# Kernel tuning notes

Measured on AMD Instinct MI355X. Metric: run time of the kernel, lower is better.

Reference implementation:

```python
import jax, jax.numpy as jnp
import numpy as np

B, S, DM, TD, H, HD = 2, 2048, 1024, 1024, 16, 64


def setup_inputs() -> dict:
    key = jax.random.key(0)
    k1, k2, k3, k4 = jax.random.split(key, 4)
    query = jax.random.normal(k1, (B, S, DM), dtype=jnp.float32)
    # fused QKV projection weight (nn.Linear weight layout: [out, in]) and output proj
    W_in = jax.random.normal(k2, (3 * TD, DM), dtype=jnp.float32) * 0.02
    W_out = jax.random.normal(k3, (DM, TD), dtype=jnp.float32) * 0.02
    # standard RoPE tables, broadcastable against [B, H, S, HD]
    inv_freq = 1.0 / (10000.0 ** (jnp.arange(0, HD, 2, dtype=jnp.float32) / HD))
    t = jnp.arange(S, dtype=jnp.float32)
    freqs = jnp.outer(t, inv_freq)                      # [S, HD/2]
    emb = jnp.concatenate([freqs, freqs], axis=-1)      # [S, HD]
    sin_q = jnp.sin(emb)[None, None]                    # [1,1,S,HD]
    cos_q = jnp.cos(emb)[None, None]
    # padding mask over keys: first length[b] positions valid (>= S/2 so no NaN rows)
    lengths = jax.random.randint(k4, (B,), S // 2, S + 1)
    attn_mask = jnp.arange(S)[None, :] < lengths[:, None]  # [B, S] bool
    return {"query": query, "W_in": W_in, "W_out": W_out,
            "sin_q": sin_q, "cos_q": cos_q, "attn_mask": attn_mask}


def _rotate_half(x):
    x1, x2 = jnp.split(x, 2, axis=-1)
    return jnp.concatenate([-x2, x1], axis=-1)


def reference(query, W_in, W_out, sin_q, cos_q, attn_mask):
    # fused QKV projection (proj_in, bias=False)
    qkv = query @ W_in.T                                # [B, S, 3*TD]
    q, k, v = jnp.split(qkv, 3, axis=-1)
    to_heads = lambda x: x.reshape(B, S, H, HD).transpose(0, 2, 1, 3)  # [B,H,S,HD]
    q, k, v = to_heads(q), to_heads(k), to_heads(v)
    # RoPE (prefix = 0 since sin covers full sequence)
    q = q * cos_q + _rotate_half(q) * sin_q
    k = k * cos_q + _rotate_half(k) * sin_q
    # SDPA with padding-mask bias + causal mask
    scale = 1.0 / jnp.sqrt(jnp.float32(HD))
    scores = jnp.einsum('bhqd,bhkd->bhqk', q, k) * scale  # [B,H,S,S]
    causal = jnp.arange(S)[:, None] >= jnp.arange(S)[None, :]  # [S, S]
    mask = attn_mask[:, None, None, :] & causal[None, None]    # [B,1,S,S]
    scores = jnp.where(mask, scores, -jnp.inf)
    attn = jax.nn.softmax(scores, axis=-1)
    out = jnp.einsum('bhqk,bhkd->bhqd', attn, v)        # [B,H,S,HD]
    out = out.transpose(0, 2, 1, 3).reshape(B, S, TD)
    return out @ W_out.T                                 # [B, S, DM]
```

## Files before the change

kernel.cpp:

```cpp
#include <hip/hip_runtime.h>
#include <hip/hip_bf16.h>

#define B_ 2
#define S_ 2048
#define DM_ 1024
#define TD_ 1024
#define H_ 16
#define HD_ 64

using bf16 = __hip_bfloat16;
typedef __attribute__((ext_vector_type(8))) short s8v;
typedef __attribute__((ext_vector_type(4))) float f4v;

__device__ __forceinline__ f4v mfma_bf16(s8v a, s8v b, f4v c) {
    return __builtin_amdgcn_mfma_f32_16x16x32_bf16(a, b, c, 0, 0, 0);
}

__device__ __forceinline__ unsigned cvt_pk_bf16(float a, float b) {
    unsigned r;
    asm("v_cvt_pk_bf16_f32 %0, %1, %2" : "=v"(r) : "v"(a), "v"(b));
    return r;
}
__device__ __forceinline__ int2 pack4bf(float a, float b, float c, float d) {
    int2 r;
    r.x = (int)cvt_pk_bf16(a, b);
    r.y = (int)cvt_pk_bf16(c, d);
    return r;
}

__device__ __forceinline__ bool detect_f32(const unsigned int* __restrict__ cosw) {
    return (cosw[0] & 0xFFFFu) == 0u;
}

__device__ __forceinline__ float ld_f(const void* p, int idx, bool f32) {
    return f32 ? ((const float*)p)[idx]
               : __bfloat162float(((const bf16*)p)[idx]);
}

__device__ __forceinline__ void gload_lds16(const bf16* g, void* l) {
    __builtin_amdgcn_global_load_lds(
        (const __attribute__((address_space(1))) unsigned int*)(const void*)g,
        (__attribute__((address_space(3))) unsigned int*)l,
        16, 0, 0);
}

#define NQ_  (B_ * S_ * DM_)
#define NWI_ (3 * TD_ * DM_)
#define NWO_ (DM_ * TD_)
#define NCVT_BLOCKS ((NQ_ + NWI_ + NWO_) / 2048)

__global__ __launch_bounds__(256)
void prep_all(const void* __restrict__ q, const void* __restrict__ wi,
              const void* __restrict__ wo, bf16* __restrict__ dst,
              const void* __restrict__ mask, int* __restrict__ lengths,
              const unsigned int* __restrict__ cosw) {
    const int bid = blockIdx.x;
    if (bid < NCVT_BLOCKS) {
        const bool f32 = detect_f32(cosw);
        int i = (bid * 256 + threadIdx.x) * 8;
        const void* src; int off;
        if (i < NQ_)              { src = q;  off = i; }
        else if (i < NQ_ + NWI_)  { src = wi; off = i - NQ_; }
        else                      { src = wo; off = i - NQ_ - NWI_; }
        if (f32) {
            const float* p = (const float*)src + off;
            float4 x = *reinterpret_cast<const float4*>(p);
            float4 y = *reinterpret_cast<const float4*>(p + 4);
            union { unsigned u[4]; int4 v; } t;
            t.u[0] = cvt_pk_bf16(x.x, x.y);
            t.u[1] = cvt_pk_bf16(x.z, x.w);
            t.u[2] = cvt_pk_bf16(y.x, y.y);
            t.u[3] = cvt_pk_bf16(y.z, y.w);
            *reinterpret_cast<int4*>(dst + i) = t.v;
        } else {
            *reinterpret_cast<int4*>(dst + i) =
                *reinterpret_cast<const int4*>((const bf16*)src + off);
        }
        return;
    }
    int b = bid - NCVT_BLOCKS;
    unsigned int w0 = ((const unsigned int*)mask)[0];
    int enc;
    if (w0 == 1u) enc = 0;
    else if (w0 == 0x01010101u) enc = 1;
    else if (w0 == 0x3F803F80u) enc = 2;
    else enc = 3;
    int cnt = 0;
    for (int s = threadIdx.x; s < S_; s += 256) {
        int i = b * S_ + s;
        bool v;
        if (enc == 0)      v = ((const int*)mask)[i] != 0;
        else if (enc == 1) v = ((const unsigned char*)mask)[i] != 0;
        else if (enc == 2) v = ((const unsigned short*)mask)[i] != 0;
        else               v = ((const float*)mask)[i] != 0.f;
        cnt += v ? 1 : 0;
    }
    __shared__ int red[256];
    red[threadIdx.x] = cnt;
    __syncthreads();
    for (int off = 128; off > 0; off >>= 1) {
        if (threadIdx.x < off) red[threadIdx.x] += red[threadIdx.x + off];
        __syncthreads();
    }
    if (threadIdx.x == 0) lengths[b] = red[0];
}

__global__ __launch_bounds__(256)
void gemm_nt(const bf16* __restrict__ A, const bf16* __restrict__ Bm,
             void* __restrict__ C, int M, int N, int K,
             int c_dyn, const unsigned int* __restrict__ cosw) {
    __shared__ bf16 lds_a[128 * 64];
    __shared__ bf16 lds_b[128 * 64];

    const bool cf32 = c_dyn && detect_f32(cosw);

    const int t = threadIdx.x;
    const int wave = t >> 6, lane = t & 63;
    const int quad = lane >> 4, l16 = lane & 15;
    const int wm = wave >> 1, wn = wave & 1;
    const int m0 = blockIdx.y * 128, n0 = blockIdx.x * 128;
    const int wuni = __builtin_amdgcn_readfirstlane(wave);

    f4v acc[4][4];
    #pragma unroll
    for (int i = 0; i < 4; i++)
        #pragma unroll
        for (int j = 0; j < 4; j++)
            acc[i][j] = f4v{0.f, 0.f, 0.f, 0.f};

    for (int k0 = 0; k0 < K; k0 += 64) {
        __syncthreads();
        #pragma unroll
        for (int i = 0; i < 4; i++) {
            int ci = i * 256 + t;
            int row = ci >> 3;
            int csrc = (ci & 7) ^ (row & 7);
            gload_lds16(A + (size_t)(m0 + row) * K + k0 + csrc * 8,
                        (char*)lds_a + i * 4096 + wuni * 1024);
            gload_lds16(Bm + (size_t)(n0 + row) * K + k0 + csrc * 8,
                        (char*)lds_b + i * 4096 + wuni * 1024);
        }
        __syncthreads();

        #pragma unroll
        for (int kk = 0; kk < 2; kk++) {
            s8v afr[4], bfr[4];
            #pragma unroll
            for (int mb = 0; mb < 4; mb++) {
                int r = wm * 64 + mb * 16 + l16;
                int ch = (kk * 4 + quad) ^ (l16 & 7);
                afr[mb] = *reinterpret_cast<const s8v*>(&lds_a[r * 64 + ch * 8]);
            }
            #pragma unroll
            for (int nb = 0; nb < 4; nb++) {
                int r = wn * 64 + nb * 16 + l16;
                int ch = (kk * 4 + quad) ^ (l16 & 7);
                bfr[nb] = *reinterpret_cast<const s8v*>(&lds_b[r * 64 + ch * 8]);
            }
            #pragma unroll
            for (int mb = 0; mb < 4; mb++)
                #pragma unroll
                for (int nb = 0; nb < 4; nb++)
                    acc[mb][nb] = mfma_bf16(bfr[nb], afr[mb], acc[mb][nb]);
        }
    }

    #pragma unroll
    for (int mb = 0; mb < 4; mb++) {
        int m = m0 + wm * 64 + mb * 16 + l16;
        #pragma unroll
        for (int nb = 0; nb < 4; nb++) {
            int n = n0 + wn * 64 + nb * 16 + quad * 4;
            f4v v = acc[mb][nb];
            if (cf32) {
                *reinterpret_cast<f4v*>(&((float*)C)[(size_t)m * N + n]) = v;
            } else {
                *reinterpret_cast<int2*>(&((bf16*)C)[(size_t)m * N + n]) =
                    pack4bf(v[0], v[1], v[2], v[3]);
            }
        }
    }
}

__global__ __launch_bounds__(256)
void rope_vt(const bf16* __restrict__ qkv,
             const void* __restrict__ sin_t, const void* __restrict__ cos_t,
             bf16* __restrict__ Qh, bf16* __restrict__ Kt, bf16* __restrict__ Vt) {
    __shared__ bf16 tile[64 * 72];
    const int bid = blockIdx.x;
    if (bid < 16384) {
        const bool f32 = detect_f32((const unsigned int*)cos_t);
        int idx = bid * 256 + threadIdx.x;
        int d = idx & 63;
        int h = (idx >> 6) & 15;
        int s = (idx >> 10) & 2047;
        int b = idx >> 21;
        size_t row = (size_t)(b * S_ + s) * 3072;
        int col  = h * 64 + d;
        int colp = h * 64 + ((d + 32) & 63);
        float sgn = (d < 32) ? -1.f : 1.f;
        float cs = ld_f(cos_t, s * 64 + d, f32);
        float sn = ld_f(sin_t, s * 64 + d, f32);
        float q  = __bfloat162float(qkv[row + col]);
        float qp = __bfloat162float(qkv[row + colp]);
        float k  = __bfloat162float(qkv[row + 1024 + col]);
        float kp = __bfloat162float(qkv[row + 1024 + colp]);
        Qh[((size_t)((b * H_ + h) * S_ + s)) * 64 + d] =
            __float2bfloat16((q * cs + sgn * qp * sn) * 0.180336880f);
        size_t ktile = ((size_t)(b * H_ + h) * 32 + (s >> 6)) * 4096;
        int dp = ((((d >> 3) ^ (s & 7)) << 3) | (d & 7));
        Kt[ktile + (s & 63) * 64 + dp] = __float2bfloat16(k * cs + sgn * kp * sn);
        return;
    }
    const int vid = bid - 16384;
    const int sb = vid & 31, h = (vid >> 5) & 15, b = vid >> 9;
    const int t = threadIdx.x;
    #pragma unroll
    for (int i = 0; i < 2; i++) {
        int id = i * 256 + t;
        int row = id >> 3, c = id & 7;
        *reinterpret_cast<int4*>(&tile[row * 72 + c * 8]) =
            *reinterpret_cast<const int4*>(
                qkv + (size_t)(b * S_ + sb * 64 + row) * 3072 + 2048 + h * 64 + c * 8);
    }
    __syncthreads();
    const size_t tb = ((size_t)(b * H_ + h) * 32 + sb) * 4096;
    #pragma unroll
    for (int i = 0; i < 2; i++) {
        int id = i * 256 + t;
        int d = id >> 3, kc = id & 7;
        union { short s[8]; int4 v; } u;
        #pragma unroll
        for (int e = 0; e < 8; e++)
            u.s[e] = reinterpret_cast<const short*>(tile)[(kc * 8 + e) * 72 + d];
        *reinterpret_cast<int4*>(Vt + tb + d * 64 + ((kc ^ (d & 7)) * 8)) = u.v;
    }
}

__global__ __launch_bounds__(256)
void attn_fused(const bf16* __restrict__ Qh, const bf16* __restrict__ Kt,
                const bf16* __restrict__ Vt, const int* __restrict__ lengths,
                bf16* __restrict__ out) {
    __shared__ bf16 k_buf[2 * 4096];
    __shared__ bf16 v_buf[2 * 4096];
    __shared__ bf16 lds_p[4 * 16 * 72];

    const int t = threadIdx.x, wave = t >> 6, lane = t & 63;
    const int quad = lane >> 4, l16 = lane & 15;
    const int bid = blockIdx.x;
    const int slot = bid >> 3;
    const int bh = (bid & 7) * 4 + (slot >> 4);
    const int p = slot & 15;
    const int b = bh >> 4, h = bh & 15;

    const size_t hb = (size_t)bh * S_ * 64;
    const bf16* Ktp = Kt + (size_t)bh * 32 * 4096;
    const bf16* Vtp = Vt + (size_t)bh * 32 * 4096;
    const int wuni = __builtin_amdgcn_readfirstlane(wave);
    int len_raw = lengths[b];
    const int len_b = len_raw < 1 ? 1 : (len_raw > S_ ? S_ : len_raw);
    const int nkt_len = (len_b + 63) >> 6;

    #pragma unroll
    for (int pass = 0; pass < 2; pass++) {
        const int qb = pass ? (31 - p) : p;
        const int qbase = qb * 64;
        const int qrow_g = qbase + wave * 16 + l16;
        const int kmax = (qrow_g < len_b - 1) ? qrow_g : (len_b - 1);

        s8v qf[2];
        {
            const bf16* qptr = Qh + hb + (size_t)qrow_g * 64 + quad * 8;
            qf[0] = *reinterpret_cast<const s8v*>(qptr);
            qf[1] = *reinterpret_cast<const s8v*>(qptr + 32);
        }

        f4v o_acc[4];
        #pragma unroll
        for (int a = 0; a < 4; a++) o_acc[a] = f4v{0.f, 0.f, 0.f, 0.f};
        float l_sum = 0.f;

        const int nkt = (qb + 1) < nkt_len ? (qb + 1) : nkt_len;

        f4v s_prev[4];
        auto process_tile = [&](int pt, const bf16* vb) {
            const int pbase = pt * 64;
            const bool tail = (pt == qb) || (pbase + 64 > len_b);
            #pragma unroll
            for (int a = 0; a < 4; a++) {
                float e0[4];
                #pragma unroll
                for (int r = 0; r < 4; r++) {
                    float e = __builtin_amdgcn_exp2f(s_prev[a][r]);
                    if (tail) {
                        int key = pbase + a * 16 + quad * 4 + r;
                        e = (key <= kmax) ? e : 0.f;
                    }
                    e0[r] = e;
                    l_sum += e;
                }
                *reinterpret_cast<int2*>(
                    &lds_p[(wave * 16 + l16) * 72 + a * 16 + quad * 4]) =
                    pack4bf(e0[0], e0[1], e0[2], e0[3]);
            }
            asm volatile("s_waitcnt lgkmcnt(0)" ::: "memory");
            #pragma unroll
            for (int kk = 0; kk < 2; kk++) {
                s8v pf = *reinterpret_cast<const s8v*>(
                    &lds_p[(wave * 16 + l16) * 72 + kk * 32 + quad * 8]);
                #pragma unroll
                for (int a = 0; a < 4; a++) {
                    int ch = (kk * 4 + quad) ^ (l16 & 7);
                    s8v vf = *reinterpret_cast<const s8v*>(
                        &vb[(a * 16 + l16) * 64 + ch * 8]);
                    o_acc[a] = mfma_bf16(vf, pf, o_acc[a]);
                }
            }
        };

        #pragma unroll
        for (int i = 0; i < 2; i++) {
            int ci = i * 256 + t;
            gload_lds16(Ktp + ci * 8, (char*)k_buf + i * 4096 + wuni * 1024);
        }
        __syncthreads();

        for (int kt = 0; kt < nkt; kt++) {
            const int cur = kt & 1;
            {
                const bf16* vst = Vtp + (size_t)kt * 4096;
                #pragma unroll
                for (int i = 0; i < 2; i++) {
                    int ci = i * 256 + t;
                    gload_lds16(vst + ci * 8,
                                (char*)v_buf + cur * 8192 + i * 4096 + wuni * 1024);
                }
            }
            if (kt + 1 < nkt) {
                const bf16* kst = Ktp + (size_t)(kt + 1) * 4096;
                #pragma unroll
                for (int i = 0; i < 2; i++) {
                    int ci = i * 256 + t;
                    gload_lds16(kst + ci * 8,
                                (char*)k_buf + (cur ^ 1) * 8192 + i * 4096 + wuni * 1024);
                }
            }

            const bf16* kb = k_buf + cur * 4096;
            f4v s_acc[4];
            #pragma unroll
            for (int a = 0; a < 4; a++) s_acc[a] = f4v{0.f, 0.f, 0.f, 0.f};
            #pragma unroll
            for (int kk = 0; kk < 2; kk++) {
                #pragma unroll
                for (int a = 0; a < 4; a++) {
                    int ch = (kk * 4 + quad) ^ (l16 & 7);
                    s8v kf = *reinterpret_cast<const s8v*>(
                        &kb[(a * 16 + l16) * 64 + ch * 8]);
                    s_acc[a] = mfma_bf16(kf, qf[kk], s_acc[a]);
                }
            }

            if (kt > 0) process_tile(kt - 1, v_buf + ((kt - 1) & 1) * 4096);

            #pragma unroll
            for (int a = 0; a < 4; a++) s_prev[a] = s_acc[a];

            __syncthreads();
        }
        process_tile(nkt - 1, v_buf + ((nkt - 1) & 1) * 4096);

        l_sum += __shfl_xor(l_sum, 16);
        l_sum += __shfl_xor(l_sum, 32);
        float inv_l = 1.f / l_sum;
        size_t orow = ((size_t)(b * S_ + qrow_g)) * TD_ + h * 64;
        #pragma unroll
        for (int a = 0; a < 4; a++) {
            *reinterpret_cast<int2*>(&out[orow + a * 16 + quad * 4]) =
                pack4bf(o_acc[a][0] * inv_l, o_acc[a][1] * inv_l,
                        o_acc[a][2] * inv_l, o_acc[a][3] * inv_l);
        }
    }
}

extern "C" void kernel_launch(void* const* d_in, const int* in_sizes, int n_in,
                              void* d_out, int out_size, void* d_ws, size_t ws_size,
                              hipStream_t stream) {
    const void* query = d_in[0];
    const void* W_in  = d_in[1];
    const void* W_out = d_in[2];
    const void* sin_q = d_in[3];
    const void* cos_q = d_in[4];
    const void* mask  = d_in[5];
    const unsigned int* cosw = (const unsigned int*)cos_q;

    const size_t nQ  = NQ_;
    const size_t nWi = NWI_;
    const size_t nWo = NWO_;

    bf16* qkv  = (bf16*)d_ws;
    bf16* Qh   = qkv + (size_t)4096 * 3072;
    bf16* Kt   = Qh + nQ;
    bf16* qbf  = Kt + nQ;
    bf16* wibf = qbf + nQ;
    bf16* wobf = wibf + nWi;
    int* lengths = (int*)(wobf + nWo);
    bf16* Vt   = qbf;
    bf16* attn = qkv;

    prep_all<<<NCVT_BLOCKS + B_, 256, 0, stream>>>(
        query, W_in, W_out, qbf, mask, lengths, cosw);

    dim3 g1(3072 / 128, 4096 / 128);
    gemm_nt<<<g1, 256, 0, stream>>>(qbf, wibf, qkv, 4096, 3072, 1024, 0, cosw);

    rope_vt<<<16384 + 1024, 256, 0, stream>>>(qkv, sin_q, cos_q, Qh, Kt, Vt);

    attn_fused<<<512, 256, 0, stream>>>(Qh, Kt, Vt, lengths, attn);

    dim3 g2(1024 / 128, 4096 / 128);
    gemm_nt<<<g2, 256, 0, stream>>>(attn, wobf, d_out, 4096, 1024, 1024, 1, cosw);
}
```

Before: 198.6 us.

## Fuse RoPE and head/V-transpose scatter into QKV GEMM epilogue

```diff
diff --git a/kernel.cpp b/kernel.cpp
--- a/kernel.cpp
+++ b/kernel.cpp
@@ -30,11 +30,6 @@
 
 __device__ __forceinline__ bool detect_f32(const unsigned int* __restrict__ cosw) {
     return (cosw[0] & 0xFFFFu) == 0u;
-}
-
-__device__ __forceinline__ float ld_f(const void* p, int idx, bool f32) {
-    return f32 ? ((const float*)p)[idx]
-               : __bfloat162float(((const bf16*)p)[idx]);
 }
 
 __device__ __forceinline__ void gload_lds16(const bf16* g, void* l) {
@@ -183,57 +178,152 @@
 }
 
 __global__ __launch_bounds__(256)
-void rope_vt(const bf16* __restrict__ qkv,
-             const void* __restrict__ sin_t, const void* __restrict__ cos_t,
-             bf16* __restrict__ Qh, bf16* __restrict__ Kt, bf16* __restrict__ Vt) {
-    __shared__ bf16 tile[64 * 72];
-    const int bid = blockIdx.x;
-    if (bid < 16384) {
+void gemm_qkv(const bf16* __restrict__ A, const bf16* __restrict__ Bm,
+              bf16* __restrict__ Qh, bf16* __restrict__ Kt, bf16* __restrict__ Vt,
+              const void* __restrict__ sin_t, const void* __restrict__ cos_t) {
+    __shared__ bf16 lds_a[128 * 64];
+    __shared__ bf16 lds_b[128 * 64];
+
+    const int t = threadIdx.x;
+    const int wave = t >> 6, lane = t & 63;
+    const int quad = lane >> 4, l16 = lane & 15;
+    const int wm = wave >> 1, wn = wave & 1;
+    const int m0 = blockIdx.y * 128, n0 = blockIdx.x * 128;
+    const int wuni = __builtin_amdgcn_readfirstlane(wave);
+
+    f4v acc[4][4];
+    #pragma unroll
+    for (int i = 0; i < 4; i++)
+        #pragma unroll
+        for (int j = 0; j < 4; j++)
+            acc[i][j] = f4v{0.f, 0.f, 0.f, 0.f};
+
+    for (int k0 = 0; k0 < 1024; k0 += 64) {
+        __syncthreads();
+        #pragma unroll
+        for (int i = 0; i < 4; i++) {
+            int ci = i * 256 + t;
+            int row = ci >> 3;
+            int csrc = (ci & 7) ^ (row & 7);
+            gload_lds16(A + (size_t)(m0 + row) * 1024 + k0 + csrc * 8,
+                        (char*)lds_a + i * 4096 + wuni * 1024);
+            gload_lds16(Bm + (size_t)(n0 + row) * 1024 + k0 + csrc * 8,
+                        (char*)lds_b + i * 4096 + wuni * 1024);
+        }
+        __syncthreads();
+
+        #pragma unroll
+        for (int kk = 0; kk < 2; kk++) {
+            s8v afr[4], bfr[4];
+            #pragma unroll
+            for (int mb = 0; mb < 4; mb++) {
+                int r = wm * 64 + mb * 16 + l16;
+                int ch = (kk * 4 + quad) ^ (l16 & 7);
+                afr[mb] = *reinterpret_cast<const s8v*>(&lds_a[r * 64 + ch * 8]);
+            }
+            #pragma unroll
+            for (int nb = 0; nb < 4; nb++) {
+                int r = wn * 64 + nb * 16 + l16;
+                int ch = (kk * 4 + quad) ^ (l16 & 7);
+                bfr[nb] = *reinterpret_cast<const s8v*>(&lds_b[r * 64 + ch * 8]);
+            }
+            #pragma unroll
+            for (int mb = 0; mb < 4; mb++)
+                #pragma unroll
+                for (int nb = 0; nb < 4; nb++)
+                    acc[mb][nb] = mfma_bf16(bfr[nb], afr[mb], acc[mb][nb]);
+        }
+    }
+
+    const int region = n0 >> 10;
+    if (region < 2) {
         const bool f32 = detect_f32((const unsigned int*)cos_t);
-        int idx = bid * 256 + threadIdx.x;
-        int d = idx & 63;
-        int h = (idx >> 6) & 15;
-        int s = (idx >> 10) & 2047;
-        int b = idx >> 21;
-        size_t row = (size_t)(b * S_ + s) * 3072;
-        int col  = h * 64 + d;
-        int colp = h * 64 + ((d + 32) & 63);
-        float sgn = (d < 32) ? -1.f : 1.f;
-        float cs = ld_f(cos_t, s * 64 + d, f32);
-        float sn = ld_f(sin_t, s * 64 + d, f32);
-        float q  = __bfloat162float(qkv[row + col]);
-        float qp = __bfloat162float(qkv[row + colp]);
-        float k  = __bfloat162float(qkv[row + 1024 + col]);
-        float kp = __bfloat162float(qkv[row + 1024 + colp]);
-        Qh[((size_t)((b * H_ + h) * S_ + s)) * 64 + d] =
-            __float2bfloat16((q * cs + sgn * qp * sn) * 0.180336880f);
-        size_t ktile = ((size_t)(b * H_ + h) * 32 + (s >> 6)) * 4096;
-        int dp = ((((d >> 3) ^ (s & 7)) << 3) | (d & 7));
-        Kt[ktile + (s & 63) * 64 + dp] = __float2bfloat16(k * cs + sgn * kp * sn);
-        return;
-    }
-    const int vid = bid - 16384;
-    const int sb = vid & 31, h = (vid >> 5) & 15, b = vid >> 9;
-    const int t = threadIdx.x;
-    #pragma unroll
-    for (int i = 0; i < 2; i++) {
-        int id = i * 256 + t;
-        int row = id >> 3, c = id & 7;
-        *reinterpret_cast<int4*>(&tile[row * 72 + c * 8]) =
-            *reinterpret_cast<const int4*>(
-                qkv + (size_t)(b * S_ + sb * 64 + row) * 3072 + 2048 + h * 64 + c * 8);
-    }
-    __syncthreads();
-    const size_t tb = ((size_t)(b * H_ + h) * 32 + sb) * 4096;
-    #pragma unroll
-    for (int i = 0; i < 2; i++) {
-        int id = i * 256 + t;
-        int d = id >> 3, kc = id & 7;
-        union { short s[8]; int4 v; } u;
-        #pragma unroll
-        for (int e = 0; e < 8; e++)
-            u.s[e] = reinterpret_cast<const short*>(tile)[(kc * 8 + e) * 72 + d];
-        *reinterpret_cast<int4*>(Vt + tb + d * 64 + ((kc ^ (d & 7)) * 8)) = u.v;
+        #pragma unroll
+        for (int mb = 0; mb < 4; mb++) {
+            const int m = m0 + wm * 64 + mb * 16 + l16;
+            const int b = m >> 11, s = m & 2047;
+            #pragma unroll
+            for (int nb = 0; nb < 4; nb++) {
+                const int n = n0 + wn * 64 + nb * 16 + quad * 4;
+                const int d = n & 63;
+                const int h = (n >> 6) & 15;
+                const float sgn = (nb < 2) ? -1.f : 1.f;
+                f4v v  = acc[mb][nb];
+                f4v vp = acc[mb][nb ^ 2];
+                float cs[4], sn[4];
+                if (f32) {
+                    float4 c4 = *reinterpret_cast<const float4*>(
+                        (const float*)cos_t + s * 64 + d);
+                    float4 s4 = *reinterpret_cast<const float4*>(
+                        (const float*)sin_t + s * 64 + d);
+                    cs[0] = c4.x; cs[1] = c4.y; cs[2] = c4.z; cs[3] = c4.w;
+                    sn[0] = s4.x; sn[1] = s4.y; sn[2] = s4.z; sn[3] = s4.w;
+                } else {
+                    const bf16* cp = (const bf16*)cos_t + s * 64 + d;
+                    const bf16* sp = (const bf16*)sin_t + s * 64 + d;
+                    #pragma unroll
+                    for (int r = 0; r < 4; r++) {
+                        cs[r] = __bfloat162float(cp[r]);
+                        sn[r] = __bfloat162float(sp[r]);
+                    }
+                }
+                float y[4];
+                #pragma unroll
+                for (int r = 0; r < 4; r++)
+                    y[r] = v[r] * cs[r] + sgn * vp[r] * sn[r];
+                if (region == 0) {
+                    size_t o = ((size_t)(b * H_ + h) * S_ + s) * 64 + d;
+                    *reinterpret_cast<int2*>(&Qh[o]) =
+                        pack4bf(y[0] * 0.180336880f, y[1] * 0.180336880f,
+                                y[2] * 0.180336880f, y[3] * 0.180336880f);
+                } else {
+                    size_t kt = ((size_t)(b * H_ + h) * 32 + (s >> 6)) * 4096;
+                    int dp = ((((d >> 3) ^ (s & 7)) << 3) | (d & 7));
+                    *reinterpret_cast<int2*>(&Kt[kt + (s & 63) * 64 + dp]) =
+                        pack4bf(y[0], y[1], y[2], y[3]);
+                }
+            }
+        }
+    } else {
+        __syncthreads();
+        bf16* half_w = (wm == 0) ? lds_a : lds_b;
+        #pragma unroll
+        for (int mb = 0; mb < 4; mb++) {
+            const int slr = mb * 16 + l16;
+            #pragma unroll
+            for (int nb = 0; nb < 4; nb++) {
+                const int nl = wn * 64 + nb * 16 + quad * 4;
+                f4v v = acc[mb][nb];
+                int off = (((nl >> 3) ^ (slr & 7)) << 3) | (nl & 7);
+                *reinterpret_cast<int2*>(&half_w[slr * 128 + off]) =
+                    pack4bf(v[0], v[1], v[2], v[3]);
+            }
+        }
+        __syncthreads();
+        const int b  = m0 >> 11;
+        const int h0 = (n0 - 2048) >> 6;
+        const int r0 = t & 7;
+        #pragma unroll
+        for (int i = 0; i < 8; i++) {
+            int id  = i * 256 + t;
+            int kc  = id & 7;
+            int d   = (id >> 3) & 63;
+            int sbl = (id >> 9) & 1;
+            int hh  = id >> 10;
+            int cb  = (hh << 3) | (d >> 3);
+            const short* half_r = reinterpret_cast<const short*>(
+                sbl ? lds_b : lds_a);
+            union { short s_[8]; int4 v4; } u;
+            #pragma unroll
+            for (int j = 0; j < 8; j++) {
+                int e   = (j + r0) & 7;
+                int slr = kc * 8 + e;
+                u.s_[e] = half_r[slr * 128 + (((cb ^ e) << 3) | (d & 7))];
+            }
+            size_t tb = ((size_t)(b * H_ + h0 + hh) * 32 +
+                         ((m0 & 2047) >> 6) + sbl) * 4096;
+            *reinterpret_cast<int4*>(&Vt[tb + d * 64 + ((kc ^ (d & 7)) << 3)]) = u.v4;
+        }
     }
 }
 
@@ -398,23 +488,21 @@
     const size_t nWi = NWI_;
     const size_t nWo = NWO_;
 
-    bf16* qkv  = (bf16*)d_ws;
-    bf16* Qh   = qkv + (size_t)4096 * 3072;
+    bf16* base = (bf16*)d_ws;
+    bf16* attn = base;
+    bf16* Vt   = base + (size_t)4096 * 1024;
+    bf16* Qh   = base + (size_t)2 * 4096 * 1024;
     bf16* Kt   = Qh + nQ;
     bf16* qbf  = Kt + nQ;
     bf16* wibf = qbf + nQ;
     bf16* wobf = wibf + nWi;
     int* lengths = (int*)(wobf + nWo);
-    bf16* Vt   = qbf;
-    bf16* attn = qkv;
 
     prep_all<<<NCVT_BLOCKS + B_, 256, 0, stream>>>(
         query, W_in, W_out, qbf, mask, lengths, cosw);
 
     dim3 g1(3072 / 128, 4096 / 128);
-    gemm_nt<<<g1, 256, 0, stream>>>(qbf, wibf, qkv, 4096, 3072, 1024, 0, cosw);
-
-    rope_vt<<<16384 + 1024, 256, 0, stream>>>(qkv, sin_q, cos_q, Qh, Kt, Vt);
+    gemm_qkv<<<g1, 256, 0, stream>>>(qbf, wibf, Qh, Kt, Vt, sin_q, cos_q);
 
     attn_fused<<<512, 256, 0, stream>>>(Qh, Kt, Vt, lengths, attn);
 
```

Result: slower. 204.3 us (+2.9%).
